# Kernel tuning notes

Measured on AMD Instinct MI355X. Metric: run time of the kernel, lower is better.

Reference implementation:

```python
import jax, jax.numpy as jnp
import numpy as np

HC = 4
C = 256
TMAX = 20
RMS_EPS = 1e-6
PRE_EPS = 0.0
SINKHORN_EPS = 1e-6
POST_MULT = 2.0


def setup_inputs() -> dict:
    key = jax.random.key(0)
    k1, k2, k3 = jax.random.split(key, 3)
    B, S = 8, 4096
    m = HC * HC + 2 * HC
    x = jax.random.normal(k1, (B, S, HC, C), dtype=jnp.float32)
    phi = jax.random.normal(k2, (HC * C, m), dtype=jnp.float32) * 0.02
    b = jnp.zeros((m,), dtype=jnp.float32)
    W = jax.random.normal(k3, (C, C), dtype=jnp.float32) * (1.0 / np.sqrt(C))
    return {
        "x": x, "phi": phi, "b": b,
        "alpha_pre": jnp.float32(1.0), "alpha_post": jnp.float32(1.0), "alpha_res": jnp.float32(1.0),
        "W": W,
    }


def _mhc_coeffs(x, phi, b, alpha_pre, alpha_post, alpha_res):
    # x: [..., HC, C] -> flatten streams, project, RMS-normalize logits.
    lead = x.shape[:-2]
    v = x.reshape(lead + (HC * C,))
    logits = jnp.einsum('...k,km->...m', v, phi)            # [..., m]
    rms = jnp.sqrt(jnp.mean(logits * logits, axis=-1, keepdims=True) + RMS_EPS)
    y = logits / rms + b                                     # [..., m]
    pre = y[..., :HC]
    post = y[..., HC:2 * HC]
    res = y[..., 2 * HC:].reshape(lead + (HC, HC))
    h_pre = jax.nn.sigmoid(alpha_pre * pre) + PRE_EPS        # [..., HC]
    h_post = POST_MULT * jax.nn.sigmoid(alpha_post * post)   # [..., HC]
    # Sinkhorn-Knopp: make exp(alpha_res * res) approximately doubly stochastic.
    P = jnp.exp(alpha_res * res)                             # [..., HC, HC]

    def step(P, _):
        P = P / (jnp.sum(P, axis=-1, keepdims=True) + SINKHORN_EPS)  # row norm
        P = P / (jnp.sum(P, axis=-2, keepdims=True) + SINKHORN_EPS)  # col norm
        return P, None

    P, _ = jax.lax.scan(step, P, None, length=TMAX)
    return h_pre, h_post, P


def reference(x, phi, b, alpha_pre, alpha_post, alpha_res, W):
    h_pre, h_post, h_res = _mhc_coeffs(x, phi, b, alpha_pre, alpha_post, alpha_res)
    # Pre-aggregate streams: x_in = sum_i h_pre[i] * x[i]
    x_in = jnp.einsum('...i,...ic->...c', h_pre, x)          # [..., C]
    # Wrapped layer: nn.Linear(C, C, bias=False) -> x_in @ W.T
    f_out = x_in @ W.T                                       # [..., C]
    # Post + residual: x_out[o] = sum_i h_res[o,i]*x[i] + h_post[o]*f_out
    x_out = jnp.einsum('...oi,...ic->...oc', h_res, x) + h_post[..., :, None] * f_out[..., None, :]
    return x_out
```

## Files before the change

kernel.cpp:

```cpp
#include <hip/hip_runtime.h>

typedef __attribute__((ext_vector_type(4))) float floatx4;
typedef __attribute__((ext_vector_type(8))) short short8;

__device__ __forceinline__ unsigned short f2bf(float f) {
    union { float f; unsigned int i; } v; v.f = f;
    unsigned int x = v.i;
    unsigned int r = (x + 0x7FFFu + ((x >> 16) & 1u)) >> 16;
    return (unsigned short)r;
}
__device__ __forceinline__ float bf2f(unsigned short u) {
    union { unsigned int i; float f; } v; v.i = ((unsigned int)u) << 16;
    return v.f;
}

__device__ __forceinline__ unsigned int cvtpk_bf16(float lo, float hi) {
    unsigned int r;
    asm("v_cvt_pk_bf16_f32 %0, %1, %2" : "=v"(r) : "v"(lo), "v"(hi));
    return r;
}

template<int CTRL>
__device__ __forceinline__ float dppf(float x) {
    return __int_as_float(__builtin_amdgcn_update_dpp(
        0, __float_as_int(x), CTRL, 0xF, 0xF, false));
}

__global__ void mhc_prep(const float* __restrict__ phi, const float* __restrict__ W,
                         unsigned short* __restrict__ phiF, unsigned short* __restrict__ WF) {
    int e = blockIdx.x * 256 + threadIdx.x;
    if (e < 32768) {
        int j = e & 7, lane = (e >> 3) & 63, nt = (e >> 9) & 1, ks = e >> 10;
        int n = nt * 16 + (lane & 15);
        int k = ks * 32 + ((lane >> 4) & 3) * 8 + j;
        float v = (n < 24) ? phi[k * 24 + n] : 0.0f;
        phiF[e] = f2bf(v);
    } else {
        int e2 = e - 32768;
        int j = e2 & 7, lane = (e2 >> 3) & 63, ks = (e2 >> 9) & 7, nt = e2 >> 12;
        int n = nt * 16 + (lane & 15);
        int k = ks * 32 + ((lane >> 4) & 3) * 8 + j;
        WF[e2] = f2bf(W[n * 256 + k]);
    }
}

#define TOK 8
#define XS_STRIDE 1032
#define XIN_STRIDE 264
#define CO_STRIDE 28

__global__ __launch_bounds__(256, 7) void mhc_main(
    const float* __restrict__ x, const float* __restrict__ bias,
    const float* __restrict__ s_ap, const float* __restrict__ s_apo,
    const float* __restrict__ s_ar,
    const unsigned short* __restrict__ phiF, const unsigned short* __restrict__ WF,
    float* __restrict__ out)
{
    __shared__ alignas(16) unsigned short xs[TOK * XS_STRIDE];
    __shared__ alignas(16) unsigned short xin_u[TOK * XIN_STRIDE];
    __shared__ alignas(16) float coef[TOK * 24];
    float* lgp = reinterpret_cast<float*>(xin_u);

    const int t = threadIdx.x;
    const int lane = t & 63;
    const int w = t >> 6;
    const int quad = lane >> 4;
    const int col = lane & 15;
    const long base = (long)blockIdx.x * (TOK * 1024);

    {
        const float4* xg = (const float4*)(x + base);
        #pragma unroll
        for (int ii = 0; ii < TOK; ++ii) {
            float4 v = xg[ii * 256 + t];
            uint2 pk;
            pk.x = cvtpk_bf16(v.x, v.y);
            pk.y = cvtpk_bf16(v.z, v.w);
            *reinterpret_cast<uint2*>(&xs[ii * XS_STRIDE + t * 4]) = pk;
        }
    }
    __syncthreads();

    {
        floatx4 acc = {0.0f, 0.0f, 0.0f, 0.0f};
        const int ntile = w & 1;
        const int kh = w >> 1;
        const int arow = col & 7;
        for (int ks = kh * 16; ks < kh * 16 + 16; ++ks) {
            short8 a = *reinterpret_cast<const short8*>(&xs[arow * XS_STRIDE + ks * 32 + quad * 8]);
            short8 b = *reinterpret_cast<const short8*>(&phiF[(ks * 2 + ntile) * 512 + lane * 8]);
            acc = __builtin_amdgcn_mfma_f32_16x16x32_bf16(a, b, acc, 0, 0, 0);
        }
        int n = ntile * 16 + col;
        if (n < 24 && quad < 2) {
            #pragma unroll
            for (int r = 0; r < 4; ++r)
                lgp[kh * (TOK * CO_STRIDE) + (quad * 4 + r) * CO_STRIDE + n] = acc[r];
        }
    }
    __syncthreads();

    if (t < 128) {
        int g = t >> 4, p = t & 15;
        const float* l0 = lgp + g * CO_STRIDE;
        const float* l1 = lgp + TOK * CO_STRIDE + g * CO_STRIDE;
        float a  = l0[p] + l1[p];
        float b2 = (p < 8) ? (l0[16 + p] + l1[16 + p]) : 0.0f;
        float s = a * a + b2 * b2;
        s += dppf<0x121>(s);
        s += dppf<0x122>(s);
        s += dppf<0x124>(s);
        s += dppf<0x128>(s);
        float rinv = 1.0f / sqrtf(s * (1.0f / 24.0f) + 1e-6f);
        float yP = (l0[8 + p] + l1[8 + p]) * rinv + bias[8 + p];
        float P = expf(s_ar[0] * yP);
        for (int it = 0; it < 20; ++it) {
            float r = P + dppf<0x39>(P);
            r += dppf<0x4E>(r);
            P *= __builtin_amdgcn_rcpf(r + 1e-6f);
            float c = P + dppf<0x124>(P);
            c += dppf<0x128>(c);
            P *= __builtin_amdgcn_rcpf(c + 1e-6f);
        }
        coef[g * 24 + 8 + p] = P;
        if (p < 8) {
            float yh = a * rinv + bias[p];
            float h = (p < 4) ? 1.0f / (1.0f + expf(-s_ap[0] * yh))
                              : 2.0f / (1.0f + expf(-s_apo[0] * yh));
            coef[g * 24 + p] = h;
        }
    }
    __syncthreads();

    {
        const int c = t;
        #pragma unroll
        for (int tok = 0; tok < TOK; ++tok) {
            float4 h4 = *reinterpret_cast<const float4*>(&coef[tok * 24]);
            const unsigned short* xr = &xs[tok * XS_STRIDE + c];
            float sv = h4.x * bf2f(xr[0]) + h4.y * bf2f(xr[256])
                     + h4.z * bf2f(xr[512]) + h4.w * bf2f(xr[768]);
            xin_u[tok * XIN_STRIDE + c] = f2bf(sv);
        }
    }
    __syncthreads();

    floatx4 accs[4];
    {
        const int arow = col & 7;
        short8 afr[8];
        #pragma unroll
        for (int ks = 0; ks < 8; ++ks)
            afr[ks] = *reinterpret_cast<const short8*>(&xin_u[arow * XIN_STRIDE + ks * 32 + quad * 8]);
        #pragma unroll
        for (int nt = 0; nt < 4; ++nt) {
            floatx4 acc = {0.0f, 0.0f, 0.0f, 0.0f};
            int ntile = w * 4 + nt;
            #pragma unroll
            for (int ks = 0; ks < 8; ++ks) {
                short8 b = *reinterpret_cast<const short8*>(&WF[(ntile * 8 + ks) * 512 + lane * 8]);
                acc = __builtin_amdgcn_mfma_f32_16x16x32_bf16(afr[ks], b, acc, 0, 0, 0);
            }
            accs[nt] = acc;
        }
    }

    {
        const int o0 = (quad >> 1) * 2;
        #pragma unroll
        for (int r = 0; r < 4; ++r) {
            int tok = (quad & 1) * 4 + r;
            const float* cb = &coef[tok * 24];
            float hpoA = cb[4 + o0], hpoB = cb[5 + o0];
            float4 PA = *reinterpret_cast<const float4*>(cb + 8 + 4 * o0);
            float4 PB = *reinterpret_cast<const float4*>(cb + 12 + 4 * o0);
            long ob = base + (long)tok * 1024 + (long)o0 * 256;
            #pragma unroll
            for (int nt = 0; nt < 4; ++nt) {
                int c = (w * 4 + nt) * 16 + col;
                float f = accs[nt][r];
                const unsigned short* xr = &xs[tok * XS_STRIDE + c];
                float x0 = bf2f(xr[0]),   x1 = bf2f(xr[256]);
                float x2 = bf2f(xr[512]), x3 = bf2f(xr[768]);
                out[ob + c]       = PA.x * x0 + PA.y * x1 + PA.z * x2 + PA.w * x3 + hpoA * f;
                out[ob + 256 + c] = PB.x * x0 + PB.y * x1 + PB.z * x2 + PB.w * x3 + hpoB * f;
            }
        }
    }
}

extern "C" void kernel_launch(void* const* d_in, const int* in_sizes, int n_in,
                              void* d_out, int out_size, void* d_ws, size_t ws_size,
                              hipStream_t stream) {
    const float* x    = (const float*)d_in[0];
    const float* phi  = (const float*)d_in[1];
    const float* bias = (const float*)d_in[2];
    const float* ap   = (const float*)d_in[3];
    const float* apo  = (const float*)d_in[4];
    const float* ar   = (const float*)d_in[5];
    const float* W    = (const float*)d_in[6];
    float* out = (float*)d_out;

    unsigned short* phiF = (unsigned short*)d_ws;
    unsigned short* WF   = (unsigned short*)d_ws + 32768;

    mhc_prep<<<384, 256, 0, stream>>>(phi, W, phiF, WF);
    mhc_main<<<4096, 256, 0, stream>>>(x, bias, ap, apo, ar, phiF, WF, out);
}
```

Baseline: 262.1 us.

## Split fused mHC kernel into front, Sinkhorn, and apply kernels

Splits the monolithic kernel into three launches. The first computes logits, RMS normalization and sigmoid gates and writes them to a workspace buffer. A per-token thread kernel then runs the Sinkhorn iterations in registers, and an apply kernel rereads x in fp32 for the pre-aggregation, GEMM and residual mix. This removes the serialized DPP Sinkhorn phase and frees LDS to raise occupancy. In exchange, x is read from global memory twice and there are extra launches.

```diff
diff --git a/kernel.cpp b/kernel.cpp
--- a/kernel.cpp
+++ b/kernel.cpp
@@ -8,10 +8,6 @@
     unsigned int x = v.i;
     unsigned int r = (x + 0x7FFFu + ((x >> 16) & 1u)) >> 16;
     return (unsigned short)r;
-}
-__device__ __forceinline__ float bf2f(unsigned short u) {
-    union { unsigned int i; float f; } v; v.i = ((unsigned int)u) << 16;
-    return v.f;
 }
 
 __device__ __forceinline__ unsigned int cvtpk_bf16(float lo, float hi) {
@@ -46,20 +42,16 @@
 
 #define TOK 8
 #define XS_STRIDE 1032
-#define XIN_STRIDE 264
 #define CO_STRIDE 28
 
-__global__ __launch_bounds__(256, 7) void mhc_main(
+__global__ __launch_bounds__(256, 8) void mhc_front(
     const float* __restrict__ x, const float* __restrict__ bias,
     const float* __restrict__ s_ap, const float* __restrict__ s_apo,
-    const float* __restrict__ s_ar,
-    const unsigned short* __restrict__ phiF, const unsigned short* __restrict__ WF,
-    float* __restrict__ out)
+    const unsigned short* __restrict__ phiF,
+    float* __restrict__ cbuf)
 {
     __shared__ alignas(16) unsigned short xs[TOK * XS_STRIDE];
-    __shared__ alignas(16) unsigned short xin_u[TOK * XIN_STRIDE];
-    __shared__ alignas(16) float coef[TOK * 24];
-    float* lgp = reinterpret_cast<float*>(xin_u);
+    __shared__ alignas(16) float lgp[2][TOK * CO_STRIDE];
 
     const int t = threadIdx.x;
     const int lane = t & 63;
@@ -95,15 +87,15 @@
         if (n < 24 && quad < 2) {
             #pragma unroll
             for (int r = 0; r < 4; ++r)
-                lgp[kh * (TOK * CO_STRIDE) + (quad * 4 + r) * CO_STRIDE + n] = acc[r];
+                lgp[kh][(quad * 4 + r) * CO_STRIDE + n] = acc[r];
         }
     }
     __syncthreads();
 
     if (t < 128) {
         int g = t >> 4, p = t & 15;
-        const float* l0 = lgp + g * CO_STRIDE;
-        const float* l1 = lgp + TOK * CO_STRIDE + g * CO_STRIDE;
+        const float* l0 = lgp[0] + g * CO_STRIDE;
+        const float* l1 = lgp[1] + g * CO_STRIDE;
         float a  = l0[p] + l1[p];
         float b2 = (p < 8) ? (l0[16 + p] + l1[16 + p]) : 0.0f;
         float s = a * a + b2 * b2;
@@ -112,35 +104,98 @@
         s += dppf<0x124>(s);
         s += dppf<0x128>(s);
         float rinv = 1.0f / sqrtf(s * (1.0f / 24.0f) + 1e-6f);
-        float yP = (l0[8 + p] + l1[8 + p]) * rinv + bias[8 + p];
-        float P = expf(s_ar[0] * yP);
-        for (int it = 0; it < 20; ++it) {
-            float r = P + dppf<0x39>(P);
-            r += dppf<0x4E>(r);
-            P *= __builtin_amdgcn_rcpf(r + 1e-6f);
-            float c = P + dppf<0x124>(P);
-            c += dppf<0x128>(c);
-            P *= __builtin_amdgcn_rcpf(c + 1e-6f);
-        }
-        coef[g * 24 + 8 + p] = P;
+        long tok = (long)blockIdx.x * TOK + g;
+        float* cb = cbuf + tok * 24;
+        cb[8 + p] = (l0[8 + p] + l1[8 + p]) * rinv + bias[8 + p];
         if (p < 8) {
             float yh = a * rinv + bias[p];
             float h = (p < 4) ? 1.0f / (1.0f + expf(-s_ap[0] * yh))
                               : 2.0f / (1.0f + expf(-s_apo[0] * yh));
-            coef[g * 24 + p] = h;
-        }
-    }
-    __syncthreads();
-
-    {
-        const int c = t;
-        #pragma unroll
-        for (int tok = 0; tok < TOK; ++tok) {
+            cb[p] = h;
+        }
+    }
+}
+
+__global__ __launch_bounds__(64) void mhc_sink(
+    float* __restrict__ cbuf, const float* __restrict__ s_ar)
+{
+    const long tok = (long)blockIdx.x * 64 + threadIdx.x;
+    float* cb = cbuf + tok * 24 + 8;
+    const float ar = s_ar[0];
+    float4 y0 = *reinterpret_cast<const float4*>(cb);
+    float4 y1 = *reinterpret_cast<const float4*>(cb + 4);
+    float4 y2 = *reinterpret_cast<const float4*>(cb + 8);
+    float4 y3 = *reinterpret_cast<const float4*>(cb + 12);
+    float p0 = expf(ar*y0.x), p1 = expf(ar*y0.y), p2 = expf(ar*y0.z), p3 = expf(ar*y0.w);
+    float p4 = expf(ar*y1.x), p5 = expf(ar*y1.y), p6 = expf(ar*y1.z), p7 = expf(ar*y1.w);
+    float p8 = expf(ar*y2.x), p9 = expf(ar*y2.y), pa = expf(ar*y2.z), pb = expf(ar*y2.w);
+    float pc = expf(ar*y3.x), pd = expf(ar*y3.y), pe = expf(ar*y3.z), pf = expf(ar*y3.w);
+    #pragma unroll
+    for (int it = 0; it < 20; ++it) {
+        float r0 = __builtin_amdgcn_rcpf(((p0+p1)+(p2+p3)) + 1e-6f);
+        float r1 = __builtin_amdgcn_rcpf(((p4+p5)+(p6+p7)) + 1e-6f);
+        float r2 = __builtin_amdgcn_rcpf(((p8+p9)+(pa+pb)) + 1e-6f);
+        float r3 = __builtin_amdgcn_rcpf(((pc+pd)+(pe+pf)) + 1e-6f);
+        p0*=r0; p1*=r0; p2*=r0; p3*=r0;
+        p4*=r1; p5*=r1; p6*=r1; p7*=r1;
+        p8*=r2; p9*=r2; pa*=r2; pb*=r2;
+        pc*=r3; pd*=r3; pe*=r3; pf*=r3;
+        float c0 = __builtin_amdgcn_rcpf(((p0+p4)+(p8+pc)) + 1e-6f);
+        float c1 = __builtin_amdgcn_rcpf(((p1+p5)+(p9+pd)) + 1e-6f);
+        float c2 = __builtin_amdgcn_rcpf(((p2+p6)+(pa+pe)) + 1e-6f);
+        float c3 = __builtin_amdgcn_rcpf(((p3+p7)+(pb+pf)) + 1e-6f);
+        p0*=c0; p4*=c0; p8*=c0; pc*=c0;
+        p1*=c1; p5*=c1; p9*=c1; pd*=c1;
+        p2*=c2; p6*=c2; pa*=c2; pe*=c2;
+        p3*=c3; p7*=c3; pb*=c3; pf*=c3;
+    }
+    float4 o0 = {p0,p1,p2,p3}, o1 = {p4,p5,p6,p7}, o2 = {p8,p9,pa,pb}, o3 = {pc,pd,pe,pf};
+    *reinterpret_cast<float4*>(cb)      = o0;
+    *reinterpret_cast<float4*>(cb + 4)  = o1;
+    *reinterpret_cast<float4*>(cb + 8)  = o2;
+    *reinterpret_cast<float4*>(cb + 12) = o3;
+}
+
+#define XIN_STRIDE 264
+
+__global__ __launch_bounds__(256, 8) void mhc_apply(
+    const float* __restrict__ x, const float* __restrict__ cbuf,
+    const unsigned short* __restrict__ WF, float* __restrict__ out)
+{
+    __shared__ alignas(16) unsigned short xin[TOK * XIN_STRIDE];
+    __shared__ alignas(16) float coef[TOK * 24];
+
+    const int t = threadIdx.x;
+    const int lane = t & 63;
+    const int w = t >> 6;
+    const int quad = lane >> 4;
+    const int col = lane & 15;
+    const long base = (long)blockIdx.x * (TOK * 1024);
+
+    if (t < 192) coef[t] = cbuf[(long)blockIdx.x * (TOK * 24) + t];
+    __syncthreads();
+
+    {
+        const int cc = (t & 63) * 4;
+        const int tok0 = w * 2;
+        #pragma unroll
+        for (int s = 0; s < 2; ++s) {
+            int tok = tok0 + s;
             float4 h4 = *reinterpret_cast<const float4*>(&coef[tok * 24]);
-            const unsigned short* xr = &xs[tok * XS_STRIDE + c];
-            float sv = h4.x * bf2f(xr[0]) + h4.y * bf2f(xr[256])
-                     + h4.z * bf2f(xr[512]) + h4.w * bf2f(xr[768]);
-            xin_u[tok * XIN_STRIDE + c] = f2bf(sv);
+            const float* xr = x + base + tok * 1024 + cc;
+            float4 x0 = *reinterpret_cast<const float4*>(xr);
+            float4 x1 = *reinterpret_cast<const float4*>(xr + 256);
+            float4 x2 = *reinterpret_cast<const float4*>(xr + 512);
+            float4 x3 = *reinterpret_cast<const float4*>(xr + 768);
+            float4 sr;
+            sr.x = h4.x * x0.x + h4.y * x1.x + h4.z * x2.x + h4.w * x3.x;
+            sr.y = h4.x * x0.y + h4.y * x1.y + h4.z * x2.y + h4.w * x3.y;
+            sr.z = h4.x * x0.z + h4.y * x1.z + h4.z * x2.z + h4.w * x3.z;
+            sr.w = h4.x * x0.w + h4.y * x1.w + h4.z * x2.w + h4.w * x3.w;
+            uint2 pk;
+            pk.x = cvtpk_bf16(sr.x, sr.y);
+            pk.y = cvtpk_bf16(sr.z, sr.w);
+            *reinterpret_cast<uint2*>(&xin[tok * XIN_STRIDE + cc]) = pk;
         }
     }
     __syncthreads();
@@ -151,7 +206,7 @@
         short8 afr[8];
         #pragma unroll
         for (int ks = 0; ks < 8; ++ks)
-            afr[ks] = *reinterpret_cast<const short8*>(&xin_u[arow * XIN_STRIDE + ks * 32 + quad * 8]);
+            afr[ks] = *reinterpret_cast<const short8*>(&xin[arow * XIN_STRIDE + ks * 32 + quad * 8]);
         #pragma unroll
         for (int nt = 0; nt < 4; ++nt) {
             floatx4 acc = {0.0f, 0.0f, 0.0f, 0.0f};
@@ -174,14 +229,15 @@
             float hpoA = cb[4 + o0], hpoB = cb[5 + o0];
             float4 PA = *reinterpret_cast<const float4*>(cb + 8 + 4 * o0);
             float4 PB = *reinterpret_cast<const float4*>(cb + 12 + 4 * o0);
-            long ob = base + (long)tok * 1024 + (long)o0 * 256;
+            long xb = base + (long)tok * 1024;
+            long ob = xb + (long)o0 * 256;
             #pragma unroll
             for (int nt = 0; nt < 4; ++nt) {
                 int c = (w * 4 + nt) * 16 + col;
                 float f = accs[nt][r];
-                const unsigned short* xr = &xs[tok * XS_STRIDE + c];
-                float x0 = bf2f(xr[0]),   x1 = bf2f(xr[256]);
-                float x2 = bf2f(xr[512]), x3 = bf2f(xr[768]);
+                const float* xr = x + xb + c;
+                float x0 = xr[0],   x1 = xr[256];
+                float x2 = xr[512], x3 = xr[768];
                 out[ob + c]       = PA.x * x0 + PA.y * x1 + PA.z * x2 + PA.w * x3 + hpoA * f;
                 out[ob + 256 + c] = PB.x * x0 + PB.y * x1 + PB.z * x2 + PB.w * x3 + hpoB * f;
             }
@@ -203,7 +259,10 @@
 
     unsigned short* phiF = (unsigned short*)d_ws;
     unsigned short* WF   = (unsigned short*)d_ws + 32768;
+    float* cbuf = (float*)((char*)d_ws + 196608);
 
     mhc_prep<<<384, 256, 0, stream>>>(phi, W, phiF, WF);
-    mhc_main<<<4096, 256, 0, stream>>>(x, bias, ap, apo, ar, phiF, WF, out);
-}
+    mhc_front<<<4096, 256, 0, stream>>>(x, bias, ap, apo, phiF, cbuf);
+    mhc_sink<<<512, 64, 0, stream>>>(cbuf, ar);
+    mhc_apply<<<4096, 256, 0, stream>>>(x, cbuf, WF, out);
+}
```

Result: slower. 349.2 us (+33.2%).
